# Optimization experiments

Hardware: AMD Instinct MI355X
Metric: run time of the kernel (lower is better)

The kernel has to match this reference:

```python
import jax, jax.numpy as jnp
import numpy as np

T, B, VD, KD, HD, OD = 64, 256, 64, 64, 512, 4


def setup_inputs() -> dict:
    key = jax.random.key(0)
    ks = jax.random.split(key, 20)
    s = 0.05
    p = {}
    p["images"] = jax.random.normal(ks[0], (T, B, 3, 32, 32), jnp.float32)
    # encoder: Conv(3->32,k4,s2) ReLU Conv(32->64,k4,s2) ReLU Conv(64->64,k4,s2) Flatten Linear(256->VD)
    p["conv1_w"] = jax.random.normal(ks[1], (32, 3, 4, 4), jnp.float32) * s
    p["conv1_b"] = jnp.zeros((32,), jnp.float32)
    p["conv2_w"] = jax.random.normal(ks[2], (64, 32, 4, 4), jnp.float32) * s
    p["conv2_b"] = jnp.zeros((64,), jnp.float32)
    p["conv3_w"] = jax.random.normal(ks[3], (64, 64, 4, 4), jnp.float32) * s
    p["conv3_b"] = jnp.zeros((64,), jnp.float32)
    p["enc_w"] = jax.random.normal(ks[4], (VD, 256), jnp.float32) * s
    p["enc_b"] = jnp.zeros((VD,), jnp.float32)
    # LSTMCell(key_dim+1 -> hidden_dim), torch gate order i,f,g,o
    p["w_ih"] = jax.random.normal(ks[5], (4 * HD, KD + 1), jnp.float32) * s
    p["w_hh"] = jax.random.normal(ks[6], (4 * HD, HD), jnp.float32) * s
    p["b_ih"] = jnp.zeros((4 * HD,), jnp.float32)
    p["b_hh"] = jnp.zeros((4 * HD,), jnp.float32)
    p["out_w"] = jax.random.normal(ks[7], (OD, HD), jnp.float32) * s
    p["out_b"] = jnp.zeros((OD,), jnp.float32)
    p["gate_w"] = jax.random.normal(ks[8], (1, HD), jnp.float32) * s
    p["gate_b"] = jnp.zeros((1,), jnp.float32)
    p["key_w"] = jax.random.normal(ks[9], (KD, HD), jnp.float32) * s
    p["key_b"] = jnp.zeros((KD,), jnp.float32)
    p["conf_w"] = jax.random.normal(ks[10], (1, 1), jnp.float32)
    p["conf_b"] = jnp.zeros((1,), jnp.float32)
    return p


def reference(images, conv1_w, conv1_b, conv2_w, conv2_b, conv3_w, conv3_b,
              enc_w, enc_b, w_ih, w_hh, b_ih, b_hh, out_w, out_b,
              gate_w, gate_b, key_w, key_b, conf_w, conf_b):
    Tn, Bn = images.shape[0], images.shape[1]

    def conv(x, w, b, relu):
        y = jax.lax.conv_general_dilated(
            x, w, window_strides=(2, 2), padding='VALID',
            dimension_numbers=('NCHW', 'OIHW', 'NCHW'))
        y = y + b[None, :, None, None]
        return jax.nn.relu(y) if relu else y

    # Encode all timesteps at once (same math as per-step encoder calls).
    x = images.reshape((Tn * Bn, 3, 32, 32))
    x = conv(x, conv1_w, conv1_b, True)
    x = conv(x, conv2_w, conv2_b, True)
    x = conv(x, conv3_w, conv3_b, False)  # no ReLU after 3rd conv in Sequential
    z_all = (x.reshape((Tn * Bn, -1)) @ enc_w.T + enc_b).reshape((Tn, Bn, -1))

    def lstm(x, h, c):
        g = x @ w_ih.T + b_ih + h @ w_hh.T + b_hh
        i, f, gg, o = jnp.split(g, 4, axis=-1)
        c2 = jax.nn.sigmoid(f) * c + jax.nn.sigmoid(i) * jnp.tanh(gg)
        return jax.nn.sigmoid(o) * jnp.tanh(c2), c2

    HDn = w_hh.shape[1]
    KDn = key_w.shape[0]
    VDn = z_all.shape[-1]
    slots = jnp.arange(Tn)

    def step(carry, xs):
        hx, cx, kx, Mk, Mv = carry
        z, t = xs
        hx, cx = lstm(kx, hx, cx)
        y = hx @ out_w.T + out_b
        g = hx @ gate_w.T + gate_b          # (b,1)
        kw = hx @ key_w.T + key_b           # (b,KD)
        # content-addressed read over the (masked) growing memory
        sim = jnp.einsum('bnd,bd->bn', Mv, z)
        mask = (slots < t)[None, :]
        wk = jax.nn.softmax(jnp.where(mask, sim, -1e30), axis=-1)
        ck = jax.nn.sigmoid(sim[..., None] * conf_w[0, 0] + conf_b[0])  # (b,n,1)
        mem = jnp.concatenate([Mk, ck], axis=-1)                         # (b,n,KD+1)
        kx_att = jax.nn.sigmoid(g) * jnp.einsum('bn,bnd->bd', wk, mem)
        kx_new = jnp.where(t == 0, jnp.zeros_like(kx_att), kx_att)      # k0 at first step
        # gated write: append kw / z at slot t
        Mk = Mk.at[:, t, :].set(kw)
        Mv = Mv.at[:, t, :].set(z)
        return (hx, cx, kx_new, Mk, Mv), y

    init = (jnp.zeros((Bn, HDn), images.dtype),
            jnp.zeros((Bn, HDn), images.dtype),
            jnp.zeros((Bn, KDn + 1), images.dtype),
            jnp.zeros((Bn, Tn, KDn), images.dtype),
            jnp.zeros((Bn, Tn, VDn), images.dtype))
    _, ys = jax.lax.scan(step, init, (z_all, slots))
    return ys  # (T, B, output_dim)
```

## Files before the change

### kernel.cpp

```cpp
#include <hip/hip_runtime.h>
#include <math.h>


__device__ __forceinline__ float sigm(float x) { return 1.0f / (1.0f + expf(-x)); }

#define PREP_N (1187840 + 2048 + 1536 + 32768 + 65536 + 16384)
__global__ __launch_bounds__(256) void prep_kernel(
    const float* __restrict__ w_ih, const float* __restrict__ w_hh,
    const float* __restrict__ b_ih, const float* __restrict__ b_hh,
    const float* __restrict__ w1, const float* __restrict__ w2,
    const float* __restrict__ w3, const float* __restrict__ ew,
    float* __restrict__ WT, float* __restrict__ bsum,
    float* __restrict__ w1T, float* __restrict__ w2T,
    float* __restrict__ w3T, float* __restrict__ ewT)
{
  int i = blockIdx.x * 256 + threadIdx.x;
  if (i < 1187840) {
    const int r = i >> 11, c = i & 2047;
    float v;
    if (r < 65)       v = w_ih[(size_t)c * 65 + r];
    else if (r < 577) v = w_hh[(size_t)c * 512 + (r - 65)];
    else              v = 0.0f;
    WT[i] = v; return;
  }
  i -= 1187840;
  if (i < 2048) { bsum[i] = b_ih[i] + b_hh[i]; return; }
  i -= 2048;
  if (i < 1536) { const int r = i >> 5, oc = i & 31; w1T[i] = w1[oc * 48 + r]; return; }
  i -= 1536;
  if (i < 32768) { const int r = i >> 6, oc = i & 63; w2T[i] = w2[oc * 512 + r]; return; }
  i -= 32768;
  if (i < 65536) { const int r = i >> 6, oc = i & 63; w3T[i] = w3[oc * 1024 + r]; return; }
  i -= 65536;
  if (i < 16384) { const int k = i >> 6, d = i & 63; ewT[i] = ew[d * 256 + k]; return; }
}

#define ENT 192
__global__ __launch_bounds__(ENT) void conv1_kernel(
    const float* __restrict__ images,
    const float* __restrict__ w1T, const float* __restrict__ b1,
    float* __restrict__ c1g, const int s0)
{
  __shared__ __align__(16) float buf[3072];
  const int bid = blockIdx.x;
  const int tid = threadIdx.x;
  {
    const float4* src = (const float4*)(images + (size_t)(s0 + bid) * 3072);
    float4* dst = (float4*)buf;
    for (int i = tid; i < 768; i += ENT) dst[i] = src[i];
  }
  __syncthreads();

  float* outp = c1g + (size_t)bid * 7680;
  for (int s = tid; s < 360; s += ENT) {
    const int ocg  = s & 7;
    const int pg   = s >> 3;
    const int row  = pg / 3;
    const int colg = pg - row * 3;
    const int ox0  = colg * 5;
    float acc[4][5];
    #pragma unroll
    for (int o = 0; o < 4; ++o) {
      const float bb = b1[ocg * 4 + o];
      #pragma unroll
      for (int p = 0; p < 5; ++p) acc[o][p] = bb;
    }
    #pragma unroll
    for (int ic = 0; ic < 3; ++ic) {
      #pragma unroll
      for (int ky = 0; ky < 4; ++ky) {
        const int y = 2 * row + ky;
        const float* ib = &buf[ic * 1024 + y * 32 + 2 * ox0];
        float v[12];
        #pragma unroll
        for (int i = 0; i < 6; ++i) { float2 t2 = *(const float2*)(ib + 2 * i); v[2*i] = t2.x; v[2*i+1] = t2.y; }
        float w_[4][4];
        #pragma unroll
        for (int kx = 0; kx < 4; ++kx)
          *(float4*)&w_[kx][0] = *(const float4*)(w1T + (ic * 16 + ky * 4 + kx) * 32 + ocg * 4);
        #pragma unroll
        for (int o = 0; o < 4; ++o)
          #pragma unroll
          for (int p = 0; p < 5; ++p)
            acc[o][p] += w_[0][o] * v[2*p] + w_[1][o] * v[2*p+1] + w_[2][o] * v[2*p+2] + w_[3][o] * v[2*p+3];
      }
    }
    #pragma unroll
    for (int o = 0; o < 4; ++o)
      #pragma unroll
      for (int p = 0; p < 5; ++p)
        outp[(ocg * 4 + o) * 240 + row * 16 + ox0 + p] = fmaxf(acc[o][p], 0.0f);
  }
}

__global__ __launch_bounds__(ENT) void enc2_kernel(
    const float* __restrict__ c1g,
    const float* __restrict__ w2T, const float* __restrict__ b2,
    const float* __restrict__ w3T, const float* __restrict__ b3,
    const float* __restrict__ ewT, const float* __restrict__ eb,
    float* __restrict__ z_all, const int s0)
{
  __shared__ __align__(16) float c1[7680];
  __shared__ __align__(16) float buf[2368];
  const int bid = blockIdx.x;
  const int tid = threadIdx.x;

  {
    const float4* src = (const float4*)(c1g + (size_t)bid * 7680);
    float4* dst = (float4*)c1;
    for (int i = tid; i < 1920; i += ENT) dst[i] = src[i];
  }
  __syncthreads();

  {
    const int ocg = tid & 15;
    const int pg  = tid >> 4;
    const int row = pg >> 1;
    const int ox0 = (pg & 1) * 3;
    float acc[4][3];
    #pragma unroll
    for (int o = 0; o < 4; ++o) {
      const float bb = b2[ocg * 4 + o];
      acc[o][0] = bb; acc[o][1] = bb; acc[o][2] = bb;
    }
    for (int ic = 0; ic < 32; ++ic) {
      #pragma unroll
      for (int ky = 0; ky < 4; ++ky) {
        const int y = 2 * row + ky;
        const float* ib = &c1[ic * 240 + y * 16 + 2 * ox0];
        float v[8];
        #pragma unroll
        for (int i = 0; i < 4; ++i) { float2 t2 = *(const float2*)(ib + 2 * i); v[2*i] = t2.x; v[2*i+1] = t2.y; }
        float w_[4][4];
        #pragma unroll
        for (int kx = 0; kx < 4; ++kx)
          *(float4*)&w_[kx][0] = *(const float4*)(w2T + (ic * 16 + ky * 4 + kx) * 64 + ocg * 4);
        #pragma unroll
        for (int o = 0; o < 4; ++o)
          #pragma unroll
          for (int p = 0; p < 3; ++p)
            acc[o][p] += w_[0][o] * v[2*p] + w_[1][o] * v[2*p+1] + w_[2][o] * v[2*p+2] + w_[3][o] * v[2*p+3];
      }
    }
    #pragma unroll
    for (int o = 0; o < 4; ++o)
      #pragma unroll
      for (int p = 0; p < 3; ++p)
        buf[(ocg * 4 + o) * 37 + row * 6 + ox0 + p] = fmaxf(acc[o][p], 0.0f);
  }
  __syncthreads();

  {
    const int oc = tid & 63;
    const int kc = tid >> 6;
    const int k0 = (kc * 256) / 3, k1 = ((kc + 1) * 256) / 3;
    float acc[4] = {0.f, 0.f, 0.f, 0.f};
    for (int it = k0; it < k1; ++it) {
      const int ic = it >> 2;
      const int ky = it & 3;
      float v[2][6];
      #pragma unroll
      for (int oy = 0; oy < 2; ++oy) {
        const float* ib = &buf[ic * 37 + (2 * oy + ky) * 6];
        #pragma unroll
        for (int i = 0; i < 3; ++i) { float2 t2 = *(const float2*)(ib + 2 * i); v[oy][2*i] = t2.x; v[oy][2*i+1] = t2.y; }
      }
      float w_[4];
      #pragma unroll
      for (int kx = 0; kx < 4; ++kx) w_[kx] = w3T[(ic * 16 + ky * 4 + kx) * 64 + oc];
      #pragma unroll
      for (int p = 0; p < 4; ++p) {
        const int oy = p >> 1, ox = p & 1;
        acc[p] += w_[0] * v[oy][2*ox] + w_[1] * v[oy][2*ox+1] + w_[2] * v[oy][2*ox+2] + w_[3] * v[oy][2*ox+3];
      }
    }
    #pragma unroll
    for (int p = 0; p < 4; ++p) c1[kc * 260 + p * 64 + oc] = acc[p];
  }
  __syncthreads();

  for (int o = tid; o < 256; o += ENT) {
    const int oc = o >> 2, p = o & 3;
    c1[1024 + o] = b3[oc] + c1[p * 64 + oc] + c1[260 + p * 64 + oc] + c1[520 + p * 64 + oc];
  }
  __syncthreads();

  {
    const int d  = tid & 63;
    const int kc = tid >> 6;
    const int k0 = (kc * 256) / 3, k1 = ((kc + 1) * 256) / 3;
    float s = 0.0f;
    for (int k = k0; k < k1; ++k) s += ewT[k * 64 + d] * c1[1024 + k];
    c1[1536 + kc * 64 + d] = s;
  }
  __syncthreads();
  if (tid < 64) {
    z_all[(size_t)(s0 + bid) * 64 + tid] = eb[tid] + c1[1536 + tid] + c1[1600 + tid] + c1[1664 + tid];
  }
}

__global__ __launch_bounds__(ENT) void encoder_kernel(
    const float* __restrict__ images,
    const float* __restrict__ w1T, const float* __restrict__ b1,
    const float* __restrict__ w2T, const float* __restrict__ b2,
    const float* __restrict__ w3T, const float* __restrict__ b3,
    const float* __restrict__ ewT, const float* __restrict__ eb,
    float* __restrict__ z_all)
{
  __shared__ __align__(16) float c1[7744];
  __shared__ __align__(16) float buf[3072];
  const int bid = blockIdx.x;
  const int tid = threadIdx.x;
  {
    const float4* src = (const float4*)(images + (size_t)bid * 3072);
    float4* dst = (float4*)buf;
    for (int i = tid; i < 768; i += ENT) dst[i] = src[i];
  }
  __syncthreads();
  for (int s = tid; s < 360; s += ENT) {
    const int ocg  = s & 7;
    const int pg   = s >> 3;
    const int row  = pg / 3;
    const int colg = pg - row * 3;
    const int ox0  = colg * 5;
    float acc[4][5];
    #pragma unroll
    for (int o = 0; o < 4; ++o) {
      const float bb = b1[ocg * 4 + o];
      #pragma unroll
      for (int p = 0; p < 5; ++p) acc[o][p] = bb;
    }
    #pragma unroll
    for (int ic = 0; ic < 3; ++ic) {
      #pragma unroll
      for (int ky = 0; ky < 4; ++ky) {
        const int y = 2 * row + ky;
        const float* ib = &buf[ic * 1024 + y * 32 + 2 * ox0];
        float v[12];
        #pragma unroll
        for (int i = 0; i < 6; ++i) { float2 t2 = *(const float2*)(ib + 2 * i); v[2*i] = t2.x; v[2*i+1] = t2.y; }
        float w_[4][4];
        #pragma unroll
        for (int kx = 0; kx < 4; ++kx)
          *(float4*)&w_[kx][0] = *(const float4*)(w1T + (ic * 16 + ky * 4 + kx) * 32 + ocg * 4);
        #pragma unroll
        for (int o = 0; o < 4; ++o)
          #pragma unroll
          for (int p = 0; p < 5; ++p)
            acc[o][p] += w_[0][o] * v[2*p] + w_[1][o] * v[2*p+1] + w_[2][o] * v[2*p+2] + w_[3][o] * v[2*p+3];
      }
    }
    #pragma unroll
    for (int o = 0; o < 4; ++o)
      #pragma unroll
      for (int p = 0; p < 5; ++p)
        c1[(ocg * 4 + o) * 242 + row * 16 + ox0 + p] = fmaxf(acc[o][p], 0.0f);
  }
  __syncthreads();
  {
    const int ocg = tid & 15;
    const int pg  = tid >> 4;
    const int row = pg >> 1;
    const int ox0 = (pg & 1) * 3;
    float acc[4][3];
    #pragma unroll
    for (int o = 0; o < 4; ++o) {
      const float bb = b2[ocg * 4 + o];
      acc[o][0] = bb; acc[o][1] = bb; acc[o][2] = bb;
    }
    for (int ic = 0; ic < 32; ++ic) {
      #pragma unroll
      for (int ky = 0; ky < 4; ++ky) {
        const int y = 2 * row + ky;
        const float* ib = &c1[ic * 242 + y * 16 + 2 * ox0];
        float v[8];
        #pragma unroll
        for (int i = 0; i < 4; ++i) { float2 t2 = *(const float2*)(ib + 2 * i); v[2*i] = t2.x; v[2*i+1] = t2.y; }
        float w_[4][4];
        #pragma unroll
        for (int kx = 0; kx < 4; ++kx)
          *(float4*)&w_[kx][0] = *(const float4*)(w2T + (ic * 16 + ky * 4 + kx) * 64 + ocg * 4);
        #pragma unroll
        for (int o = 0; o < 4; ++o)
          #pragma unroll
          for (int p = 0; p < 3; ++p)
            acc[o][p] += w_[0][o] * v[2*p] + w_[1][o] * v[2*p+1] + w_[2][o] * v[2*p+2] + w_[3][o] * v[2*p+3];
      }
    }
    __syncthreads();
    #pragma unroll
    for (int o = 0; o < 4; ++o)
      #pragma unroll
      for (int p = 0; p < 3; ++p)
        buf[(ocg * 4 + o) * 38 + row * 6 + ox0 + p] = fmaxf(acc[o][p], 0.0f);
  }
  __syncthreads();
  {
    const int oc = tid & 63;
    const int kc = tid >> 6;
    const int k0 = (kc * 256) / 3, k1 = ((kc + 1) * 256) / 3;
    float acc[4] = {0.f, 0.f, 0.f, 0.f};
    for (int it = k0; it < k1; ++it) {
      const int ic = it >> 2;
      const int ky = it & 3;
      float v[2][6];
      #pragma unroll
      for (int oy = 0; oy < 2; ++oy) {
        const float* ib = &buf[ic * 38 + (2 * oy + ky) * 6];
        #pragma unroll
        for (int i = 0; i < 3; ++i) { float2 t2 = *(const float2*)(ib + 2 * i); v[oy][2*i] = t2.x; v[oy][2*i+1] = t2.y; }
      }
      float w_[4];
      #pragma unroll
      for (int kx = 0; kx < 4; ++kx) w_[kx] = w3T[(ic * 16 + ky * 4 + kx) * 64 + oc];
      #pragma unroll
      for (int p = 0; p < 4; ++p) {
        const int oy = p >> 1, ox = p & 1;
        acc[p] += w_[0] * v[oy][2*ox] + w_[1] * v[oy][2*ox+1] + w_[2] * v[oy][2*ox+2] + w_[3] * v[oy][2*ox+3];
      }
    }
    #pragma unroll
    for (int p = 0; p < 4; ++p) c1[kc * 260 + p * 64 + oc] = acc[p];
  }
  __syncthreads();
  for (int o = tid; o < 256; o += ENT) {
    const int oc = o >> 2, p = o & 3;
    c1[1024 + o] = b3[oc] + c1[p * 64 + oc] + c1[260 + p * 64 + oc] + c1[520 + p * 64 + oc];
  }
  __syncthreads();
  {
    const int d  = tid & 63;
    const int kc = tid >> 6;
    const int k0 = (kc * 256) / 3, k1 = ((kc + 1) * 256) / 3;
    float s = 0.0f;
    for (int k = k0; k < k1; ++k) s += ewT[k * 64 + d] * c1[1024 + k];
    c1[1536 + kc * 64 + d] = s;
  }
  __syncthreads();
  if (tid < 64) {
    z_all[(size_t)bid * 64 + tid] = eb[tid] + c1[1536 + tid] + c1[1600 + tid] + c1[1664 + tid];
  }
}

__global__ __launch_bounds__(256) void gram_kernel(
    const float* __restrict__ z_all, float* __restrict__ z_gram)
{
  const int b = blockIdx.x;
  const int tid = threadIdx.x;
  __shared__ float zsb[64 * 65];
  for (int i = tid; i < 4096; i += 256) {
    const int tt = i >> 6, d = i & 63;
    zsb[tt * 65 + d] = z_all[((size_t)tt * 256 + b) * 64 + d];
  }
  __syncthreads();
  const int n = tid & 63, tg = tid >> 6;
  for (int tt = tg; tt < 64; tt += 4) {
    float s = 0.0f;
    #pragma unroll
    for (int d = 0; d < 64; ++d) s += zsb[tt * 65 + d] * zsb[n * 65 + d];
    z_gram[((size_t)b * 64 + tt) * 64 + n] = s;
  }
}

__global__ __launch_bounds__(256) void gates_partial_kernel(
    const float* __restrict__ XC, const float* __restrict__ WT,
    float* __restrict__ Gp, const int kchunk, const int klog)
{
  extern __shared__ float xs[];
  const int bx  = blockIdx.x;
  const int kc  = bx & ((1 << klog) - 1);
  const int jt  = bx >> klog;
  const int tid = threadIdx.x;
  const int tj  = tid & 63, tb = tid >> 6;
  const int k0  = kc * kchunk;
  const int b0  = blockIdx.y * 16;
  const int j0  = jt * 256 + tj * 4;

  const int NS = 16 * kchunk;
  for (int i = tid; i < NS; i += 256) {
    const int k = i >> 4, b = i & 15;
    xs[k * 16 + b] = XC[(size_t)(b0 + b) * 580 + k0 + k];
  }
  __syncthreads();

  float acc[4][4];
  #pragma unroll
  for (int bb = 0; bb < 4; ++bb) { acc[bb][0]=0.f; acc[bb][1]=0.f; acc[bb][2]=0.f; acc[bb][3]=0.f; }

  const float* wp = WT + (size_t)k0 * 2048 + j0;
  const float* xp = xs + tb * 4;
  #pragma unroll 4
  for (int k = 0; k < kchunk; ++k) {
    const float4 w = *(const float4*)(wp + (size_t)k * 2048);
    const float4 x = *(const float4*)(xp + k * 16);
    const float xv[4] = {x.x, x.y, x.z, x.w};
    #pragma unroll
    for (int bb = 0; bb < 4; ++bb) {
      acc[bb][0] += xv[bb] * w.x; acc[bb][1] += xv[bb] * w.y;
      acc[bb][2] += xv[bb] * w.z; acc[bb][3] += xv[bb] * w.w;
    }
  }
  #pragma unroll
  for (int bb = 0; bb < 4; ++bb) {
    float4 r; r.x = acc[bb][0]; r.y = acc[bb][1]; r.z = acc[bb][2]; r.w = acc[bb][3];
    *(float4*)(Gp + ((size_t)kc * 256 + b0 + tb * 4 + bb) * 2048 + j0) = r;
  }
}

__global__ __launch_bounds__(256) void step_fused_kernel(
    const int t, const int kcn,
    const float* __restrict__ Gp, const float* __restrict__ bsum,
    float* __restrict__ C, const float* __restrict__ z_gram,
    float* __restrict__ MkT, float* __restrict__ XC, float* __restrict__ out,
    const float* __restrict__ out_w, const float* __restrict__ out_b,
    const float* __restrict__ gate_w, const float* __restrict__ gate_b,
    const float* __restrict__ key_w, const float* __restrict__ key_b,
    const float* __restrict__ conf_w, const float* __restrict__ conf_b)
{
  const int b   = blockIdx.x;
  const int tid = threadIdx.x;
  __shared__ __align__(16) float hs[512];
  __shared__ __align__(16) float wks[64];
  __shared__ __align__(16) float psum[256];
  __shared__ float sgv, kx64v;

  for (int jj = tid; jj < 512; jj += 256) {
    float gv[4];
    #pragma unroll
    for (int g = 0; g < 4; ++g) {
      float s = bsum[g * 512 + jj];
      for (int kc = 0; kc < kcn; ++kc)
        s += Gp[((size_t)kc * 256 + b) * 2048 + g * 512 + jj];
      gv[g] = s;
    }
    const size_t cidx = (size_t)b * 512 + jj;
    const float c2v = sigm(gv[1]) * C[cidx] + sigm(gv[0]) * tanhf(gv[2]);
    C[cidx] = c2v;
    const float h = sigm(gv[3]) * tanhf(c2v);
    hs[jj] = h;
    XC[(size_t)b * 580 + 65 + jj] = h;
  }
  __syncthreads();

  const int wv = tid >> 6, lane = tid & 63;
  for (int d = wv; d < 69; d += 4) {
    const float* row = (d < 64) ? (key_w + (size_t)d * 512)
                     : (d < 68) ? (out_w + (size_t)(d - 64) * 512)
                                : gate_w;
    float a = 0.0f;
    #pragma unroll
    for (int k = 0; k < 8; ++k) a += hs[lane + k * 64] * row[lane + k * 64];
    #pragma unroll
    for (int m = 32; m > 0; m >>= 1) a += __shfl_xor(a, m);
    if (lane == 0) {
      if (d < 64)      MkT[(size_t)b * 4096 + d * 64 + t] = a + key_b[d];
      else if (d < 68) out[(size_t)t * 1024 + b * 4 + (d - 64)] = a + out_b[d - 64];
      else             sgv = sigm(a + gate_b[0]);
    }
  }
  __syncthreads();

  if (t == 0) {
    if (tid < 65) XC[(size_t)b * 580 + tid] = 0.0f;
    return;
  }

  if (tid < 64) {
    const int n = tid;
    const float sim = z_gram[((size_t)b * 64 + t) * 64 + n];
    const bool valid = (n < t);
    float mx = valid ? sim : -3.0e38f;
    #pragma unroll
    for (int m = 32; m > 0; m >>= 1) mx = fmaxf(mx, __shfl_xor(mx, m));
    const float p = valid ? expf(sim - mx) : 0.0f;
    float sum = p;
    #pragma unroll
    for (int m = 32; m > 0; m >>= 1) sum += __shfl_xor(sum, m);
    const float wk = p / sum;
    wks[n] = wk;
    float kcv = wk * sigm(sim * conf_w[0] + conf_b[0]);
    #pragma unroll
    for (int m = 32; m > 0; m >>= 1) kcv += __shfl_xor(kcv, m);
    if (n == 0) kx64v = kcv;
  }
  __syncthreads();

  {
    const int d = tid >> 2, q = tid & 3;
    const float* mr = MkT + (size_t)b * 4096 + d * 64 + q * 16;
    const float* wr = wks + q * 16;
    float a = 0.0f;
    #pragma unroll
    for (int i = 0; i < 4; ++i) {
      const float4 m4 = *(const float4*)(mr + 4 * i);
      const float4 w4 = *(const float4*)(wr + 4 * i);
      a += m4.x * w4.x + m4.y * w4.y + m4.z * w4.z + m4.w * w4.w;
    }
    psum[tid] = a;
  }
  __syncthreads();
  if (tid < 64) {
    XC[(size_t)b * 580 + tid] = sgv * (psum[tid * 4] + psum[tid * 4 + 1] + psum[tid * 4 + 2] + psum[tid * 4 + 3]);
  } else if (tid == 64) {
    XC[(size_t)b * 580 + 64] = sgv * kx64v;
  }
}

extern "C" void kernel_launch(void* const* d_in, const int* in_sizes, int n_in,
                              void* d_out, int out_size, void* d_ws, size_t ws_size,
                              hipStream_t stream) {
  const float* images = (const float*)d_in[0];
  const float* w1     = (const float*)d_in[1];
  const float* b1     = (const float*)d_in[2];
  const float* w2     = (const float*)d_in[3];
  const float* b2     = (const float*)d_in[4];
  const float* w3     = (const float*)d_in[5];
  const float* b3     = (const float*)d_in[6];
  const float* ew     = (const float*)d_in[7];
  const float* eb     = (const float*)d_in[8];
  const float* w_ih   = (const float*)d_in[9];
  const float* w_hh   = (const float*)d_in[10];
  const float* b_ih   = (const float*)d_in[11];
  const float* b_hh   = (const float*)d_in[12];
  const float* out_w  = (const float*)d_in[13];
  const float* out_b  = (const float*)d_in[14];
  const float* gate_w = (const float*)d_in[15];
  const float* gate_b = (const float*)d_in[16];
  const float* key_w  = (const float*)d_in[17];
  const float* key_b  = (const float*)d_in[18];
  const float* conf_w = (const float*)d_in[19];
  const float* conf_b = (const float*)d_in[20];
  float* out = (float*)d_out;
  float* ws  = (float*)d_ws;

  float* WT     = ws;
  float* bsum   = ws + 1187840;
  float* w1T    = ws + 1189888;
  float* w2T    = ws + 1191424;
  float* w3T    = ws + 1224192;
  float* ewT    = ws + 1289728;
  float* z_all  = ws + 1306112;
  float* MkT    = ws + 2354688;
  float* C      = ws + 3403264;
  float* XC     = ws + 3534336;
  float* z_gram = ws + 3682816;
  float* Gp     = ws + 4731392;

  int kcn = 4, klog = 2, kchunk = 145;
  if (ws_size < (4731392ull + 4ull * 524288ull) * 4ull) { kcn = 2; klog = 1; kchunk = 290; }
  if (ws_size < (4731392ull + 2ull * 524288ull) * 4ull) { kcn = 1; klog = 0; kchunk = 580; }

  const size_t baseF  = 4731392ull + (size_t)kcn * 524288ull;
  float* c1g          = ws + baseF;
  const size_t availF = (ws_size / 4 > baseF) ? (ws_size / 4 - baseF) : 0;
  long chunkL = (long)(availF / 7680ull);
  int chunk = (chunkL > 16384) ? 16384 : (int)chunkL;

  hipMemsetAsync(C,  0, 131072 * sizeof(float), stream);
  hipMemsetAsync(XC, 0, 148480 * sizeof(float), stream);

  prep_kernel<<<(PREP_N + 255) / 256, 256, 0, stream>>>(
      w_ih, w_hh, b_ih, b_hh, w1, w2, w3, ew, WT, bsum, w1T, w2T, w3T, ewT);

  if (chunk >= 2048) {
    for (int s0 = 0; s0 < 16384; s0 += chunk) {
      const int n = (16384 - s0 < chunk) ? (16384 - s0) : chunk;
      conv1_kernel<<<n, ENT, 0, stream>>>(images, w1T, b1, c1g, s0);
      enc2_kernel<<<n, ENT, 0, stream>>>(c1g, w2T, b2, w3T, b3, ewT, eb, z_all, s0);
    }
  } else {
    encoder_kernel<<<16384, ENT, 0, stream>>>(images, w1T, b1, w2T, b2, w3T, b3, ewT, eb, z_all);
  }

  gram_kernel<<<256, 256, 0, stream>>>(z_all, z_gram);

  const size_t lds_stage = (size_t)16 * kchunk * sizeof(float);
  for (int t = 0; t < 64; ++t) {
    gates_partial_kernel<<<dim3(8 * kcn, 16), 256, lds_stage, stream>>>(
        XC, WT, Gp, kchunk, klog);
    step_fused_kernel<<<256, 256, 0, stream>>>(
        t, kcn, Gp, bsum, C, z_gram, MkT, XC, out,
        out_w, out_b, gate_w, gate_b, key_w, key_b, conf_w, conf_b);
  }
}
```

Baseline: 4.191 ms.

## Fuse per-step gate GEMM and LSTM cell/attention into a single scan kernel

Merges the split-K gate GEMM and the per-batch step kernel into one kernel per timestep. Each block owns a 16-batch tile and a 128-column gate slice: it recomputes the LSTM cell update for its tile, computes key/out/gate projections and the attention read, and then produces the next step's gate pre-activations into a ping-pong buffer. The aim is to halve kernel launches, drop the split-K partial-sum pass, and keep the concatenated input in LDS instead of global memory. In exchange, the cell update and Gin reads are repeated redundantly across 16 blocks, and the GEMM uses a smaller per-thread tile.

Result: slower. 11.93 ms (+184.8%).

```diff
diff --git a/kernel.cpp b/kernel.cpp
--- a/kernel.cpp
+++ b/kernel.cpp
@@ -362,147 +362,128 @@
   }
 }
 
-__global__ __launch_bounds__(256) void gates_partial_kernel(
-    const float* __restrict__ XC, const float* __restrict__ WT,
-    float* __restrict__ Gp, const int kchunk, const int klog)
-{
-  extern __shared__ float xs[];
-  const int bx  = blockIdx.x;
-  const int kc  = bx & ((1 << klog) - 1);
-  const int jt  = bx >> klog;
-  const int tid = threadIdx.x;
-  const int tj  = tid & 63, tb = tid >> 6;
-  const int k0  = kc * kchunk;
-  const int b0  = blockIdx.y * 16;
-  const int j0  = jt * 256 + tj * 4;
-
-  const int NS = 16 * kchunk;
-  for (int i = tid; i < NS; i += 256) {
-    const int k = i >> 4, b = i & 15;
-    xs[k * 16 + b] = XC[(size_t)(b0 + b) * 580 + k0 + k];
-  }
-  __syncthreads();
-
-  float acc[4][4];
-  #pragma unroll
-  for (int bb = 0; bb < 4; ++bb) { acc[bb][0]=0.f; acc[bb][1]=0.f; acc[bb][2]=0.f; acc[bb][3]=0.f; }
-
-  const float* wp = WT + (size_t)k0 * 2048 + j0;
-  const float* xp = xs + tb * 4;
-  #pragma unroll 4
-  for (int k = 0; k < kchunk; ++k) {
-    const float4 w = *(const float4*)(wp + (size_t)k * 2048);
-    const float4 x = *(const float4*)(xp + k * 16);
-    const float xv[4] = {x.x, x.y, x.z, x.w};
-    #pragma unroll
-    for (int bb = 0; bb < 4; ++bb) {
-      acc[bb][0] += xv[bb] * w.x; acc[bb][1] += xv[bb] * w.y;
-      acc[bb][2] += xv[bb] * w.z; acc[bb][3] += xv[bb] * w.w;
-    }
-  }
-  #pragma unroll
-  for (int bb = 0; bb < 4; ++bb) {
-    float4 r; r.x = acc[bb][0]; r.y = acc[bb][1]; r.z = acc[bb][2]; r.w = acc[bb][3];
-    *(float4*)(Gp + ((size_t)kc * 256 + b0 + tb * 4 + bb) * 2048 + j0) = r;
-  }
-}
-
-__global__ __launch_bounds__(256) void step_fused_kernel(
-    const int t, const int kcn,
-    const float* __restrict__ Gp, const float* __restrict__ bsum,
-    float* __restrict__ C, const float* __restrict__ z_gram,
-    float* __restrict__ MkT, float* __restrict__ XC, float* __restrict__ out,
+__global__ __launch_bounds__(256) void scan_step_kernel(
+    const int t,
+    const float* __restrict__ Gin, float* __restrict__ Gout,
+    const float* __restrict__ bsum,
+    const float* __restrict__ Cin, float* __restrict__ Cout,
+    const float* __restrict__ z_gram, float* __restrict__ MkT,
+    float* __restrict__ out, const float* __restrict__ WT,
     const float* __restrict__ out_w, const float* __restrict__ out_b,
     const float* __restrict__ gate_w, const float* __restrict__ gate_b,
     const float* __restrict__ key_w, const float* __restrict__ key_b,
     const float* __restrict__ conf_w, const float* __restrict__ conf_b)
 {
-  const int b   = blockIdx.x;
+  __shared__ __align__(16) float xsT[577 * 18];
+  __shared__ __align__(16) float wks[16 * 64];
+  __shared__ float sgs[16], kx64s[16];
+
+  const int bx  = blockIdx.x;
+  const int bt  = bx >> 4;
+  const int jt  = bx & 15;
+  const int b0  = bt * 16;
   const int tid = threadIdx.x;
-  __shared__ __align__(16) float hs[512];
-  __shared__ __align__(16) float wks[64];
-  __shared__ __align__(16) float psum[256];
-  __shared__ float sgv, kx64v;
-
-  for (int jj = tid; jj < 512; jj += 256) {
+  const int lane = tid & 63, wid = tid >> 6;
+
+  for (int i = tid; i < 16 * 512; i += 256) {
+    const int b = i >> 9, j = i & 511;
     float gv[4];
     #pragma unroll
     for (int g = 0; g < 4; ++g) {
-      float s = bsum[g * 512 + jj];
-      for (int kc = 0; kc < kcn; ++kc)
-        s += Gp[((size_t)kc * 256 + b) * 2048 + g * 512 + jj];
+      float s = bsum[g * 512 + j];
+      if (t > 0) s += Gin[(size_t)(b0 + b) * 2048 + g * 512 + j];
       gv[g] = s;
     }
-    const size_t cidx = (size_t)b * 512 + jj;
-    const float c2v = sigm(gv[1]) * C[cidx] + sigm(gv[0]) * tanhf(gv[2]);
-    C[cidx] = c2v;
-    const float h = sigm(gv[3]) * tanhf(c2v);
-    hs[jj] = h;
-    XC[(size_t)b * 580 + 65 + jj] = h;
-  }
-  __syncthreads();
-
-  const int wv = tid >> 6, lane = tid & 63;
-  for (int d = wv; d < 69; d += 4) {
+    const size_t cidx = (size_t)(b0 + b) * 512 + j;
+    const float c2v = sigm(gv[1]) * Cin[cidx] + sigm(gv[0]) * tanhf(gv[2]);
+    Cout[cidx] = c2v;
+    xsT[(65 + j) * 18 + b] = sigm(gv[3]) * tanhf(c2v);
+  }
+  __syncthreads();
+
+  for (int task = wid; task < 96; task += 4) {
+    const int dd = task >> 4, b = task & 15;
+    if (dd == 4 && jt >= 4) continue;
+    const int d = (dd < 4) ? dd * 16 + jt : ((dd == 4) ? 64 + jt : 68);
     const float* row = (d < 64) ? (key_w + (size_t)d * 512)
                      : (d < 68) ? (out_w + (size_t)(d - 64) * 512)
                                 : gate_w;
     float a = 0.0f;
     #pragma unroll
-    for (int k = 0; k < 8; ++k) a += hs[lane + k * 64] * row[lane + k * 64];
+    for (int kk = 0; kk < 8; ++kk)
+      a += xsT[(65 + lane + kk * 64) * 18 + b] * row[lane + kk * 64];
     #pragma unroll
     for (int m = 32; m > 0; m >>= 1) a += __shfl_xor(a, m);
     if (lane == 0) {
-      if (d < 64)      MkT[(size_t)b * 4096 + d * 64 + t] = a + key_b[d];
-      else if (d < 68) out[(size_t)t * 1024 + b * 4 + (d - 64)] = a + out_b[d - 64];
-      else             sgv = sigm(a + gate_b[0]);
+      if (d < 64)      MkT[(size_t)(b0 + b) * 4096 + d * 64 + t] = a + key_b[d];
+      else if (d < 68) out[(size_t)t * 1024 + (b0 + b) * 4 + (d - 64)] = a + out_b[d - 64];
+      else             sgs[b] = sigm(a + gate_b[0]);
+    }
+  }
+
+  if (t > 0) {
+    const float cw = conf_w[0], cb = conf_b[0];
+    for (int b = wid; b < 16; b += 4) {
+      const float sim = z_gram[((size_t)(b0 + b) * 64 + t) * 64 + lane];
+      const bool valid = (lane < t);
+      float mx = valid ? sim : -3.0e38f;
+      #pragma unroll
+      for (int m = 32; m > 0; m >>= 1) mx = fmaxf(mx, __shfl_xor(mx, m));
+      const float p = valid ? expf(sim - mx) : 0.0f;
+      float sum = p;
+      #pragma unroll
+      for (int m = 32; m > 0; m >>= 1) sum += __shfl_xor(sum, m);
+      const float wk = p / sum;
+      wks[b * 64 + lane] = wk;
+      float kc = wk * sigm(sim * cw + cb);
+      #pragma unroll
+      for (int m = 32; m > 0; m >>= 1) kc += __shfl_xor(kc, m);
+      if (lane == 0) kx64s[b] = kc;
     }
   }
   __syncthreads();
 
   if (t == 0) {
-    if (tid < 65) XC[(size_t)b * 580 + tid] = 0.0f;
-    return;
-  }
-
-  if (tid < 64) {
-    const int n = tid;
-    const float sim = z_gram[((size_t)b * 64 + t) * 64 + n];
-    const bool valid = (n < t);
-    float mx = valid ? sim : -3.0e38f;
-    #pragma unroll
-    for (int m = 32; m > 0; m >>= 1) mx = fmaxf(mx, __shfl_xor(mx, m));
-    const float p = valid ? expf(sim - mx) : 0.0f;
-    float sum = p;
-    #pragma unroll
-    for (int m = 32; m > 0; m >>= 1) sum += __shfl_xor(sum, m);
-    const float wk = p / sum;
-    wks[n] = wk;
-    float kcv = wk * sigm(sim * conf_w[0] + conf_b[0]);
-    #pragma unroll
-    for (int m = 32; m > 0; m >>= 1) kcv += __shfl_xor(kcv, m);
-    if (n == 0) kx64v = kcv;
-  }
-  __syncthreads();
-
-  {
-    const int d = tid >> 2, q = tid & 3;
-    const float* mr = MkT + (size_t)b * 4096 + d * 64 + q * 16;
-    const float* wr = wks + q * 16;
-    float a = 0.0f;
-    #pragma unroll
-    for (int i = 0; i < 4; ++i) {
-      const float4 m4 = *(const float4*)(mr + 4 * i);
-      const float4 w4 = *(const float4*)(wr + 4 * i);
-      a += m4.x * w4.x + m4.y * w4.y + m4.z * w4.z + m4.w * w4.w;
-    }
-    psum[tid] = a;
-  }
-  __syncthreads();
-  if (tid < 64) {
-    XC[(size_t)b * 580 + tid] = sgv * (psum[tid * 4] + psum[tid * 4 + 1] + psum[tid * 4 + 2] + psum[tid * 4 + 3]);
-  } else if (tid == 64) {
-    XC[(size_t)b * 580 + 64] = sgv * kx64v;
+    for (int i = tid; i < 65 * 16; i += 256) xsT[(i >> 4) * 18 + (i & 15)] = 0.0f;
+  } else {
+    const int d = tid & 63, bg = tid >> 6;
+    #pragma unroll
+    for (int ii = 0; ii < 4; ++ii) {
+      const int b = bg * 4 + ii;
+      const float* mr = MkT + (size_t)(b0 + b) * 4096 + d * 64;
+      const float* wr = wks + b * 64;
+      float a = 0.0f;
+      #pragma unroll
+      for (int q = 0; q < 16; ++q) {
+        const float4 m4 = *(const float4*)(mr + 4 * q);
+        const float4 w4 = *(const float4*)(wr + 4 * q);
+        a += m4.x * w4.x + m4.y * w4.y + m4.z * w4.z + m4.w * w4.w;
+      }
+      xsT[d * 18 + b] = sgs[b] * a;
+    }
+    if (tid < 16) xsT[64 * 18 + tid] = sgs[tid] * kx64s[tid];
+  }
+  __syncthreads();
+
+  {
+    const int tj = tid & 31, tb = tid >> 5;
+    const int j0 = jt * 128 + tj * 4;
+    float acc[2][4];
+    #pragma unroll
+    for (int i = 0; i < 2; ++i) { acc[i][0]=0.f; acc[i][1]=0.f; acc[i][2]=0.f; acc[i][3]=0.f; }
+    const float* wp = WT + j0;
+    #pragma unroll 4
+    for (int k = 0; k < 577; ++k) {
+      const float4 w = *(const float4*)(wp + (size_t)k * 2048);
+      const float2 x = *(const float2*)(&xsT[k * 18 + tb * 2]);
+      acc[0][0] += x.x * w.x; acc[0][1] += x.x * w.y; acc[0][2] += x.x * w.z; acc[0][3] += x.x * w.w;
+      acc[1][0] += x.y * w.x; acc[1][1] += x.y * w.y; acc[1][2] += x.y * w.z; acc[1][3] += x.y * w.w;
+    }
+    #pragma unroll
+    for (int i = 0; i < 2; ++i) {
+      float4 r; r.x = acc[i][0]; r.y = acc[i][1]; r.z = acc[i][2]; r.w = acc[i][3];
+      *(float4*)(Gout + (size_t)(b0 + tb * 2 + i) * 2048 + j0) = r;
+    }
   }
 }
 
@@ -541,23 +522,18 @@
   float* ewT    = ws + 1289728;
   float* z_all  = ws + 1306112;
   float* MkT    = ws + 2354688;
-  float* C      = ws + 3403264;
-  float* XC     = ws + 3534336;
-  float* z_gram = ws + 3682816;
-  float* Gp     = ws + 4731392;
-
-  int kcn = 4, klog = 2, kchunk = 145;
-  if (ws_size < (4731392ull + 4ull * 524288ull) * 4ull) { kcn = 2; klog = 1; kchunk = 290; }
-  if (ws_size < (4731392ull + 2ull * 524288ull) * 4ull) { kcn = 1; klog = 0; kchunk = 580; }
-
-  const size_t baseF  = 4731392ull + (size_t)kcn * 524288ull;
-  float* c1g          = ws + baseF;
+  float* C0     = ws + 3403264;
+  float* C1     = ws + 3534336;
+  float* z_gram = ws + 3665408;
+  float* G0     = ws + 4713984;
+  float* G1     = ws + 5238272;
+  const size_t baseF = 5762560;
+  float* c1g = ws + baseF;
   const size_t availF = (ws_size / 4 > baseF) ? (ws_size / 4 - baseF) : 0;
   long chunkL = (long)(availF / 7680ull);
   int chunk = (chunkL > 16384) ? 16384 : (int)chunkL;
 
-  hipMemsetAsync(C,  0, 131072 * sizeof(float), stream);
-  hipMemsetAsync(XC, 0, 148480 * sizeof(float), stream);
+  hipMemsetAsync(C0, 0, 131072 * sizeof(float), stream);
 
   prep_kernel<<<(PREP_N + 255) / 256, 256, 0, stream>>>(
       w_ih, w_hh, b_ih, b_hh, w1, w2, w3, ew, WT, bsum, w1T, w2T, w3T, ewT);
@@ -574,12 +550,13 @@
 
   gram_kernel<<<256, 256, 0, stream>>>(z_all, z_gram);
 
-  const size_t lds_stage = (size_t)16 * kchunk * sizeof(float);
   for (int t = 0; t < 64; ++t) {
-    gates_partial_kernel<<<dim3(8 * kcn, 16), 256, lds_stage, stream>>>(
-        XC, WT, Gp, kchunk, klog);
-    step_fused_kernel<<<256, 256, 0, stream>>>(
-        t, kcn, Gp, bsum, C, z_gram, MkT, XC, out,
+    const float* Gin  = (t & 1) ? G1 : G0;
+    float*       Gout = (t & 1) ? G0 : G1;
+    const float* Cin  = (t & 1) ? C1 : C0;
+    float*       Cout = (t & 1) ? C0 : C1;
+    scan_step_kernel<<<256, 256, 0, stream>>>(
+        t, Gin, Gout, bsum, Cin, Cout, z_gram, MkT, out, WT,
         out_w, out_b, gate_w, gate_b, key_w, key_b, conf_w, conf_b);
   }
 }
```
